# Performance work log

Hardware: AMD Instinct MI355X
Metric: run time of the kernel (lower is better)

## Reference

```python
import jax, jax.numpy as jnp
import numpy as np

VOCAB = 50000
SEQ = 2048
BATCH = 64
D = 256


def setup_inputs() -> dict:
    key = jax.random.key(0)
    ks = jax.random.split(key, 9)
    x = jax.random.randint(ks[0], (SEQ, BATCH), 0, VOCAB)  # token ids, 0 = pad
    emb = jax.random.normal(ks[1], (VOCAB, D), jnp.float32) * 0.02
    emb = emb.at[0].set(0.0)  # padding_idx=0
    idf = jax.random.uniform(ks[2], (VOCAB,), jnp.float32, 0.1, 10.0)
    W1 = jax.random.normal(ks[3], (100, D), jnp.float32) * (1.0 / np.sqrt(D))
    b1 = jax.random.normal(ks[4], (100,), jnp.float32) * 0.01
    W2 = jax.random.normal(ks[5], (150, 100), jnp.float32) * 0.1
    b2 = jax.random.normal(ks[6], (150,), jnp.float32) * 0.01
    W3 = jax.random.normal(ks[7], (2, 150), jnp.float32) * 0.1
    b3 = jax.random.normal(ks[8], (2,), jnp.float32) * 0.01
    return {"x": x, "emb": emb, "idf": idf, "W1": W1, "b1": b1,
            "W2": W2, "b2": b2, "W3": W3, "b3": b3}


def reference(x, emb, idf, W1, b1, W2, b2, W3, b3):
    tokens = x.T  # [B, S] (nums = x.permute(1, 0))
    vocab = emb.shape[0]

    # per-row term frequency: histogram (scatter-add) then gather back
    def tf_row(row):  # row: [S] int
        return jnp.zeros((vocab,), jnp.float32).at[row].add(1.0)[row]

    tf = jax.vmap(tf_row)(tokens)                      # [B, S]
    scores = jnp.where(tokens == 0, 0.0, tf * idf[tokens])  # [B, S]

    # bmm of (B, D, S) with (B, S, 1) == tf-idf weighted sum of embeddings
    pooled = jnp.einsum('bsd,bs->bd', emb[tokens], scores)  # [B, D]

    h = jax.nn.relu(pooled @ W1.T + b1)
    h = jax.nn.relu(h @ W2.T + b2)
    return jax.nn.softmax(h @ W3.T + b3, axis=-1)  # [B, 2]
```

## Files before the change

### kernel.cpp

```cpp
#include <hip/hip_runtime.h>

#define VOCAB 50000
#define SEQ   2048
#define BATCH 64
#define DIM   256
#define H1    100
#define H2    150
#define HASH  4096
#define NW    16

__global__ __launch_bounds__(1024)
void k_fused(const int* __restrict__ x,
             const float* __restrict__ emb,
             const float* __restrict__ idf,
             const float* __restrict__ W1, const float* __restrict__ b1,
             const float* __restrict__ W2, const float* __restrict__ b2,
             const float* __restrict__ W3, const float* __restrict__ b3,
             float* __restrict__ out) {
    __shared__ int   tok[SEQ];
    __shared__ int   hkey[HASH];
    __shared__ int   hcnt[HASH];
    __shared__ float sc[SEQ];
    __shared__ float wacc[NW][DIM];
    __shared__ float pooled[DIM];
    __shared__ float hp1[128][4];
    __shared__ float h1s[H1];
    __shared__ float hp2[H2][4];
    __shared__ float h2s[H2];
    __shared__ float lg[2];

    const int b = blockIdx.x;
    const int t = threadIdx.x;
    const int w = t >> 6, lane = t & 63;

    for (int i = t; i < HASH; i += 1024) { hkey[i] = -1; hcnt[i] = 0; }
#pragma unroll
    for (int n = 0; n < SEQ / 1024; ++n) {
        const int s = n * 1024 + t;
        tok[s] = x[s * BATCH + b];
    }
    __syncthreads();

#pragma unroll
    for (int n = 0; n < SEQ / 1024; ++n) {
        const int s = n * 1024 + t;
        const int mytok = tok[s];
        unsigned h = ((unsigned)mytok * 2654435761u) >> 20;
        while (true) {
            int prev = atomicCAS(&hkey[h], -1, mytok);
            if (prev == -1 || prev == mytok) { atomicAdd(&hcnt[h], 1); break; }
            h = (h + 1) & (HASH - 1);
        }
    }
    __syncthreads();

#pragma unroll
    for (int n = 0; n < SEQ / 1024; ++n) {
        const int s = n * 1024 + t;
        const int mytok = tok[s];
        unsigned h = ((unsigned)mytok * 2654435761u) >> 20;
        while (hkey[h] != mytok) h = (h + 1) & (HASH - 1);
        sc[s] = (mytok == 0) ? 0.0f : (float)hcnt[h] * idf[mytok];
    }
    __syncthreads();

    {
        const float4* embv = (const float4*)emb;
        float4 acc = make_float4(0.f, 0.f, 0.f, 0.f);
        const int s0 = w * (SEQ / NW);
#pragma unroll 4
        for (int i = 0; i < SEQ / NW; ++i) {
            const int s = s0 + i;
            const float sv = sc[s];
            const float4 v = embv[(size_t)tok[s] * (DIM / 4) + lane];
            acc.x = fmaf(v.x, sv, acc.x);
            acc.y = fmaf(v.y, sv, acc.y);
            acc.z = fmaf(v.z, sv, acc.z);
            acc.w = fmaf(v.w, sv, acc.w);
        }
        ((float4*)wacc[w])[lane] = acc;
    }
    __syncthreads();

    if (t < DIM) {
        float a = 0.0f;
#pragma unroll
        for (int i = 0; i < NW; ++i) a += wacc[i][t];
        pooled[t] = a;
    }
    __syncthreads();

    if (t < 512) {
        const int j = t >> 2;
        const int q = t & 3;
        if (j < H1) {
            const float4* wv = (const float4*)(W1 + j * DIM + q * 64);
            const float4* pv = (const float4*)(pooled) + q * 16;
            float a = 0.0f;
#pragma unroll
            for (int i = 0; i < 16; ++i) {
                const float4 ww = wv[i];
                const float4 pp = pv[i];
                a += ww.x * pp.x + ww.y * pp.y + ww.z * pp.z + ww.w * pp.w;
            }
            hp1[j][q] = a;
        }
    }
    __syncthreads();
    if (t < H1)
        h1s[t] = fmaxf(hp1[t][0] + hp1[t][1] + hp1[t][2] + hp1[t][3] + b1[t], 0.0f);
    __syncthreads();

    if (t < 600) {
        const int j = t >> 2;
        const int q = t & 3;
        const float* wv = W2 + j * H1 + q * 25;
        float a = 0.0f;
#pragma unroll
        for (int i = 0; i < 25; ++i)
            a = fmaf(wv[i], h1s[q * 25 + i], a);
        hp2[j][q] = a;
    }
    __syncthreads();
    if (t < H2)
        h2s[t] = fmaxf(hp2[t][0] + hp2[t][1] + hp2[t][2] + hp2[t][3] + b2[t], 0.0f);
    __syncthreads();

    if (t < 2) {
        const float* wv = W3 + t * H2;
        float a = b3[t];
        for (int k = 0; k < H2; ++k) a = fmaf(wv[k], h2s[k], a);
        lg[t] = a;
    }
    __syncthreads();
    if (t == 0) {
        const float m  = fmaxf(lg[0], lg[1]);
        const float e0 = __expf(lg[0] - m);
        const float e1 = __expf(lg[1] - m);
        const float inv = 1.0f / (e0 + e1);
        out[b * 2 + 0] = e0 * inv;
        out[b * 2 + 1] = e1 * inv;
    }
}

extern "C" void kernel_launch(void* const* d_in, const int* in_sizes, int n_in,
                              void* d_out, int out_size, void* d_ws, size_t ws_size,
                              hipStream_t stream) {
    const int*   x   = (const int*)  d_in[0];
    const float* emb = (const float*)d_in[1];
    const float* idf = (const float*)d_in[2];
    const float* W1  = (const float*)d_in[3];
    const float* b1  = (const float*)d_in[4];
    const float* W2  = (const float*)d_in[5];
    const float* b2  = (const float*)d_in[6];
    const float* W3  = (const float*)d_in[7];
    const float* b3  = (const float*)d_in[8];
    float* out = (float*)d_out;

    k_fused<<<BATCH, 1024, 0, stream>>>(x, emb, idf, W1, b1, W2, b2, W3, b3, out);
}
```

Baseline: 129.4 us.

## Split each batch row across eight blocks with last-block reduction

Launches BATCH*8 blocks instead of BATCH, so each block gathers and weights only one eighth of the sequence's embeddings. Per-chunk partial sums go to workspace, and an atomic counter picks the last block per row to reduce the partials and run the MLP and softmax. This fills more of the GPU's compute units for the memory-bound gather. In exchange, every block still rebuilds the full-row hash histogram, and the change adds a memset, global partial writes, and fence/atomic synchronization.

```diff
diff --git a/kernel.cpp b/kernel.cpp
--- a/kernel.cpp
+++ b/kernel.cpp
@@ -7,43 +7,52 @@
 #define H1    100
 #define H2    150
 #define HASH  4096
-#define NW    16
+#define NCH   8
+#define CHUNK (SEQ / NCH)
+#define NT    1024
+#define NWAVE (NT / 64)
 
 __global__ __launch_bounds__(1024)
-void k_fused(const int* __restrict__ x,
-             const float* __restrict__ emb,
-             const float* __restrict__ idf,
-             const float* __restrict__ W1, const float* __restrict__ b1,
-             const float* __restrict__ W2, const float* __restrict__ b2,
-             const float* __restrict__ W3, const float* __restrict__ b3,
-             float* __restrict__ out) {
+void k_main(const int* __restrict__ x,
+            const float* __restrict__ emb,
+            const float* __restrict__ idf,
+            const float* __restrict__ W1, const float* __restrict__ b1,
+            const float* __restrict__ W2, const float* __restrict__ b2,
+            const float* __restrict__ W3, const float* __restrict__ b3,
+            unsigned* __restrict__ counters,
+            float* __restrict__ partials,
+            float* __restrict__ out) {
     __shared__ int   tok[SEQ];
     __shared__ int   hkey[HASH];
     __shared__ int   hcnt[HASH];
-    __shared__ float sc[SEQ];
-    __shared__ float wacc[NW][DIM];
+    __shared__ float sc[CHUNK];
+    __shared__ float wacc[NWAVE][DIM];
     __shared__ float pooled[DIM];
     __shared__ float hp1[128][4];
-    __shared__ float h1s[H1];
+    __shared__ float h1s[112];
     __shared__ float hp2[H2][4];
-    __shared__ float h2s[H2];
+    __shared__ float h2s[152];
     __shared__ float lg[2];
+    __shared__ int   isLast;
 
-    const int b = blockIdx.x;
-    const int t = threadIdx.x;
-    const int w = t >> 6, lane = t & 63;
+    const int bx = blockIdx.x;
+    const int r  = bx >> 3;
+    const int c  = bx & (NCH - 1);
+    const int t  = threadIdx.x;
+    const int w  = t >> 6, lane = t & 63;
+    const int s0 = c * CHUNK;
 
-    for (int i = t; i < HASH; i += 1024) { hkey[i] = -1; hcnt[i] = 0; }
+    for (int i = t; i < HASH; i += NT) { hkey[i] = -1; hcnt[i] = 0; }
 #pragma unroll
-    for (int n = 0; n < SEQ / 1024; ++n) {
-        const int s = n * 1024 + t;
-        tok[s] = x[s * BATCH + b];
+    for (int n = 0; n < SEQ / NT; ++n) {
+        const int s = n * NT + t;
+        tok[s] = x[s * BATCH + r];
     }
     __syncthreads();
 
 #pragma unroll
-    for (int n = 0; n < SEQ / 1024; ++n) {
-        const int s = n * 1024 + t;
+    for (int n = 0; n < SEQ / NT; ++n) {
+        const int s = n * NT + t;
         const int mytok = tok[s];
         unsigned h = ((unsigned)mytok * 2654435761u) >> 20;
         while (true) {
@@ -54,25 +63,23 @@
     }
     __syncthreads();
 
-#pragma unroll
-    for (int n = 0; n < SEQ / 1024; ++n) {
-        const int s = n * 1024 + t;
+    if (t < CHUNK) {
+        const int s = s0 + t;
         const int mytok = tok[s];
         unsigned h = ((unsigned)mytok * 2654435761u) >> 20;
         while (hkey[h] != mytok) h = (h + 1) & (HASH - 1);
-        sc[s] = (mytok == 0) ? 0.0f : (float)hcnt[h] * idf[mytok];
+        sc[t] = (mytok == 0) ? 0.0f : (float)hcnt[h] * idf[mytok];
     }
     __syncthreads();
 
     {
         const float4* embv = (const float4*)emb;
         float4 acc = make_float4(0.f, 0.f, 0.f, 0.f);
-        const int s0 = w * (SEQ / NW);
-#pragma unroll 4
-        for (int i = 0; i < SEQ / NW; ++i) {
-            const int s = s0 + i;
-            const float sv = sc[s];
-            const float4 v = embv[(size_t)tok[s] * (DIM / 4) + lane];
+        const int i0 = w * (CHUNK / NWAVE);
+#pragma unroll
+        for (int i = 0; i < CHUNK / NWAVE; ++i) {
+            const float sv = sc[i0 + i];
+            const float4 v = embv[(size_t)tok[s0 + i0 + i] * (DIM / 4) + lane];
             acc.x = fmaf(v.x, sv, acc.x);
             acc.y = fmaf(v.y, sv, acc.y);
             acc.z = fmaf(v.z, sv, acc.z);
@@ -85,7 +92,25 @@
     if (t < DIM) {
         float a = 0.0f;
 #pragma unroll
-        for (int i = 0; i < NW; ++i) a += wacc[i][t];
+        for (int i = 0; i < NWAVE; ++i) a += wacc[i][t];
+        partials[(size_t)bx * DIM + t] = a;
+        __threadfence();
+    }
+    __syncthreads();
+    if (t == 0) {
+        unsigned prev = atomicAdd(&counters[r], 1u);
+        isLast = (prev == NCH - 1);
+    }
+    __syncthreads();
+    if (!isLast) return;
+
+    __threadfence();
+
+    if (t < DIM) {
+        float a = 0.0f;
+#pragma unroll
+        for (int cc = 0; cc < NCH; ++cc)
+            a += partials[((size_t)r * NCH + cc) * DIM + t];
         pooled[t] = a;
     }
     __syncthreads();
@@ -95,7 +120,7 @@
         const int q = t & 3;
         if (j < H1) {
             const float4* wv = (const float4*)(W1 + j * DIM + q * 64);
-            const float4* pv = (const float4*)(pooled) + q * 16;
+            const float4* pv = ((const float4*)pooled) + q * 16;
             float a = 0.0f;
 #pragma unroll
             for (int i = 0; i < 16; ++i) {
@@ -138,8 +163,8 @@
         const float e0 = __expf(lg[0] - m);
         const float e1 = __expf(lg[1] - m);
         const float inv = 1.0f / (e0 + e1);
-        out[b * 2 + 0] = e0 * inv;
-        out[b * 2 + 1] = e1 * inv;
+        out[r * 2 + 0] = e0 * inv;
+        out[r * 2 + 1] = e1 * inv;
     }
 }
 
@@ -157,5 +182,10 @@
     const float* b3  = (const float*)d_in[8];
     float* out = (float*)d_out;
 
-    k_fused<<<BATCH, 1024, 0, stream>>>(x, emb, idf, W1, b1, W2, b2, W3, b3, out);
+    unsigned* counters = (unsigned*)d_ws;
+    float*    partials = (float*)((char*)d_ws + 1024);
+
+    hipMemsetAsync(counters, 0, BATCH * sizeof(unsigned), stream);
+    k_main<<<BATCH * NCH, NT, 0, stream>>>(x, emb, idf, W1, b1, W2, b2, W3, b3,
+                                           counters, partials, out);
 }
```

New measurement: 289.5 us. 124% more time.
